# Optimization experiments

Measured on AMD Instinct MI355X. Metric: run time of the kernel, lower is better.

The kernel has to match this reference:

```python
import jax, jax.numpy as jnp
import numpy as np

N_QUBITS = 4
N_LAYERS = 2


def _ry(theta):
    # PennyLane RY(theta) = [[cos(t/2), -sin(t/2)], [sin(t/2), cos(t/2)]]
    c = jnp.cos(theta / 2)
    s = jnp.sin(theta / 2)
    return jnp.stack([jnp.stack([c, -s]), jnp.stack([s, c])]).astype(jnp.complex64)


def _rz(theta):
    # PennyLane RZ(theta) = diag(exp(-i t/2), exp(+i t/2))
    e = jnp.exp(-0.5j * theta.astype(jnp.complex64))
    return jnp.diag(jnp.stack([e, jnp.conj(e)]))


def _apply_1q(state, U, wire):
    # state: (2,)*N_QUBITS complex; contract U into axis `wire`
    state = jnp.tensordot(U, state, axes=((1,), (wire,)))
    return jnp.moveaxis(state, 0, wire)


def _cnot(state, ctrl, tgt):
    s = jnp.moveaxis(state, ctrl, 0)
    t2 = tgt - 1 if tgt > ctrl else tgt
    s1 = jnp.flip(s[1], axis=t2)  # X on target where control == 1
    return jnp.moveaxis(jnp.stack([s[0], s1]), 0, ctrl)


def _circuit(angles, weights):
    # angles: (N_QUBITS,), weights: (N_LAYERS, N_QUBITS, 2)
    state = jnp.zeros((2,) * N_QUBITS, jnp.complex64).at[(0,) * N_QUBITS].set(1.0)
    for i in range(N_QUBITS):
        state = _apply_1q(state, _ry(angles[i]), i)
    for l in range(N_LAYERS):
        for i in range(N_QUBITS):
            state = _apply_1q(state, _ry(weights[l, i, 0]), i)
            state = _apply_1q(state, _rz(weights[l, i, 1]), i)
        for i in range(N_QUBITS - 1):
            state = _cnot(state, i, i + 1)
        state = _cnot(state, N_QUBITS - 1, 0)
    probs = jnp.abs(state) ** 2
    p = probs.reshape(2, -1).sum(axis=1)  # marginal on wire 0
    return p[0] - p[1]  # <Z_0>


def setup_inputs() -> dict:
    key = jax.random.key(0)
    ks = jax.random.split(key, 6)
    B = 65536
    return {
        "x": jax.random.normal(ks[0], (B, 256), jnp.float32),
        "W1": jax.random.normal(ks[1], (64, 256), jnp.float32) * 0.0625,
        "b1": jax.random.normal(ks[2], (64,), jnp.float32) * 0.01,
        "W2": jax.random.normal(ks[3], (4, 64), jnp.float32) * 0.125,
        "b2": jax.random.normal(ks[4], (4,), jnp.float32) * 0.01,
        "q_weights": jax.random.normal(ks[5], (N_LAYERS, N_QUBITS, 2), jnp.float32) * 0.1,
    }


def reference(x, W1, b1, W2, b2, q_weights):
    h = jax.nn.relu(x @ W1.T + b1)          # [B, 64]
    angles = jnp.tanh(h @ W2.T + b2)         # [B, 4]
    z = jax.vmap(lambda a: _circuit(a, q_weights))(angles)  # [B]
    return z[:, None]                        # [B, 1]
```

## Files before the change

kernel.cpp:

```cpp
#include <hip/hip_runtime.h>
#include <math.h>

typedef _Float16 half8  __attribute__((ext_vector_type(8)));
typedef _Float16 half4v __attribute__((ext_vector_type(4)));
typedef float    float4v __attribute__((ext_vector_type(4)));

#define BM   128
#define KDIM 256
#define BKF  128
#define XSTR 136
#define HSW  65

__global__ __launch_bounds__(256, 2)
void qc_fused(const float* __restrict__ x,
              const float* __restrict__ W1,
              const float* __restrict__ b1,
              const float* __restrict__ W2,
              const float* __restrict__ b2,
              const float* __restrict__ qw,
              float* __restrict__ out)
{
    __shared__ _Float16 xh[BM * XSTR];
    __shared__ _Float16 wh[64 * XSTR];
    __shared__ float w2s[256];
    __shared__ float b1s[64];
    __shared__ float b2s[4];
    __shared__ float trig[32];

    const int tid  = threadIdx.x;
    const int lane = tid & 63;
    const int wv   = tid >> 6;
    const int m    = lane & 15;
    const int q    = lane >> 4;
    const int row0 = blockIdx.x * BM;

    w2s[tid] = W2[tid];
    if (tid < 64) b1s[tid] = b1[tid];
    if (tid < 4)  b2s[tid] = b2[tid];
    if (tid < 8) {
        int l = tid >> 2, i = tid & 3;
        float wy = qw[(l * 4 + i) * 2 + 0];
        float wz = qw[(l * 4 + i) * 2 + 1];
        float sy, cy, sz, cz;
        sincosf(0.5f * wy, &sy, &cy);
        sincosf(0.5f * wz, &sz, &cz);
        trig[(l * 4 + i) * 4 + 0] = cy;
        trig[(l * 4 + i) * 4 + 1] = sy;
        trig[(l * 4 + i) * 4 + 2] = cz;
        trig[(l * 4 + i) * 4 + 3] = sz;
    }

    float4v acc[2][4] = {};

    const int sr  = tid >> 3, skq = tid & 7;
    const int wr  = tid >> 2, wkq = tid & 3;

    for (int kc = 0; kc < KDIM; kc += BKF) {
        if (kc) __syncthreads();
        #pragma unroll
        for (int i = 0; i < 4; ++i) {
            #pragma unroll
            for (int j = 0; j < 4; ++j) {
                int row = sr + 32 * i;
                int kf  = 4 * skq + 32 * j;
                const float4v v = *(const float4v*)(x + (size_t)(row0 + row) * KDIM + kc + kf);
                half4v h;
                h[0] = (_Float16)v[0]; h[1] = (_Float16)v[1];
                h[2] = (_Float16)v[2]; h[3] = (_Float16)v[3];
                *(half4v*)&xh[row * XSTR + kf] = h;
            }
        }
        #pragma unroll
        for (int j = 0; j < 8; ++j) {
            int kf = 4 * wkq + 16 * j;
            const float4v v = *(const float4v*)(W1 + (size_t)wr * KDIM + kc + kf);
            half4v h;
            h[0] = (_Float16)v[0]; h[1] = (_Float16)v[1];
            h[2] = (_Float16)v[2]; h[3] = (_Float16)v[3];
            *(half4v*)&wh[wr * XSTR + kf] = h;
        }
        __syncthreads();
        #pragma unroll
        for (int ks = 0; ks < 4; ++ks) {
            const int ko = ks * 32 + q * 8;
            half8 af0 = *(const half8*)&xh[(wv * 32 +      m) * XSTR + ko];
            half8 af1 = *(const half8*)&xh[(wv * 32 + 16 + m) * XSTR + ko];
            #pragma unroll
            for (int b = 0; b < 4; ++b) {
                half8 bf = *(const half8*)&wh[(16 * b + m) * XSTR + ko];
                acc[0][b] = __builtin_amdgcn_mfma_f32_16x16x32_f16(af0, bf, acc[0][b], 0, 0, 0);
                acc[1][b] = __builtin_amdgcn_mfma_f32_16x16x32_f16(af1, bf, acc[1][b], 0, 0, 0);
            }
        }
    }
    __syncthreads();

    float* hs = (float*)xh;
    #pragma unroll
    for (int a = 0; a < 2; ++a) {
        #pragma unroll
        for (int b = 0; b < 4; ++b) {
            #pragma unroll
            for (int i = 0; i < 4; ++i) {
                int row = wv * 32 + 16 * a + 4 * q + i;
                int col = 16 * b + m;
                float v = acc[a][b][i] + b1s[col];
                hs[row * HSW + col] = fmaxf(v, 0.0f);
            }
        }
    }
    __syncthreads();

    if (tid < BM) {
        const int r = tid;
        float s0 = b2s[0], s1 = b2s[1], s2 = b2s[2], s3 = b2s[3];
        #pragma unroll 8
        for (int k = 0; k < 64; ++k) {
            float hv = hs[r * HSW + k];
            s0 = fmaf(hv, w2s[0 * 64 + k], s0);
            s1 = fmaf(hv, w2s[1 * 64 + k], s1);
            s2 = fmaf(hv, w2s[2 * 64 + k], s2);
            s3 = fmaf(hv, w2s[3 * 64 + k], s3);
        }
        float ang[4] = { tanhf(s0), tanhf(s1), tanhf(s2), tanhf(s3) };

        float ca[4], sa[4];
        #pragma unroll
        for (int i = 0; i < 4; ++i)
            __sincosf(0.5f * ang[i], &sa[i], &ca[i]);

        float re[16], im[16];
        #pragma unroll
        for (int idx = 0; idx < 16; ++idx) {
            re[idx] = (idx & 8 ? sa[0] : ca[0]) * (idx & 4 ? sa[1] : ca[1]) *
                      (idx & 2 ? sa[2] : ca[2]) * (idx & 1 ? sa[3] : ca[3]);
            im[idx] = 0.0f;
        }
        #pragma unroll
        for (int l = 0; l < 2; ++l) {
            #pragma unroll
            for (int i = 0; i < 4; ++i) {
                const float cy = trig[(l * 4 + i) * 4 + 0];
                const float sy = trig[(l * 4 + i) * 4 + 1];
                const float cz = trig[(l * 4 + i) * 4 + 2];
                const float sz = trig[(l * 4 + i) * 4 + 3];
                const int mq = 8 >> i;
                #pragma unroll
                for (int idx = 0; idx < 16; ++idx) {
                    if (!(idx & mq)) {
                        int j = idx | mq;
                        float ar = re[idx], ai = im[idx], br = re[j], bi = im[j];
                        re[idx] = fmaf(cy, ar, -sy * br);
                        im[idx] = fmaf(cy, ai, -sy * bi);
                        re[j]   = fmaf(sy, ar,  cy * br);
                        im[j]   = fmaf(sy, ai,  cy * bi);
                    }
                }
                #pragma unroll
                for (int idx = 0; idx < 16; ++idx) {
                    float sgn = (idx & mq) ? sz : -sz;
                    float ar = re[idx], ai = im[idx];
                    re[idx] = fmaf(ar, cz, -ai * sgn);
                    im[idx] = fmaf(ar, sgn, ai * cz);
                }
            }
            #pragma unroll
            for (int c = 0; c < 4; ++c) {
                int t  = (c + 1) & 3;
                int mc = 8 >> c, mt = 8 >> t;
                #pragma unroll
                for (int idx = 0; idx < 16; ++idx) {
                    if ((idx & mc) && !(idx & mt)) {
                        int j = idx | mt;
                        float tr = re[idx]; re[idx] = re[j]; re[j] = tr;
                        float ti = im[idx]; im[idx] = im[j]; im[j] = ti;
                    }
                }
            }
        }
        float z = 0.0f;
        #pragma unroll
        for (int idx = 0; idx < 16; ++idx) {
            float p = re[idx] * re[idx] + im[idx] * im[idx];
            z += (idx & 8) ? -p : p;
        }
        out[row0 + r] = z;
    }
}

extern "C" void kernel_launch(void* const* d_in, const int* in_sizes, int n_in,
                              void* d_out, int out_size, void* d_ws, size_t ws_size,
                              hipStream_t stream) {
    const float* x  = (const float*)d_in[0];
    const float* W1 = (const float*)d_in[1];
    const float* b1 = (const float*)d_in[2];
    const float* W2 = (const float*)d_in[3];
    const float* b2 = (const float*)d_in[4];
    const float* qw = (const float*)d_in[5];
    float* out = (float*)d_out;
    const int B = in_sizes[0] / KDIM;
    qc_fused<<<B / BM, 256, 0, stream>>>(x, W1, b1, W2, b2, qw, out);
}
```

Before: 104.5 us.

## Load x straight into MFMA A-fragments, shrink tile to 64 rows, split second layer across threads

Each wave now reads its 16 rows of x directly from global memory into registers as fp16 A-fragments, so x no longer passes through shared memory. W1 is staged once with the full K, which removes the two-chunk K loop. The block tile shrinks to 64 rows, shared memory is aliased between W1 and the hidden buffer, and occupancy is raised to 4 blocks per SM. The second linear layer is split so all 256 threads each compute one output angle instead of 128 threads computing four. This trades more blocks, and more W1 reloads per row of output, for fewer LDS round trips and fewer idle threads.

Result: slower. 107.6 us (+3.0%).

```diff
diff --git a/kernel.cpp b/kernel.cpp
--- a/kernel.cpp
+++ b/kernel.cpp
@@ -1,17 +1,16 @@
 #include <hip/hip_runtime.h>
 #include <math.h>
 
-typedef _Float16 half8  __attribute__((ext_vector_type(8)));
-typedef _Float16 half4v __attribute__((ext_vector_type(4)));
+typedef _Float16 half8   __attribute__((ext_vector_type(8)));
+typedef _Float16 half4v  __attribute__((ext_vector_type(4)));
 typedef float    float4v __attribute__((ext_vector_type(4)));
 
-#define BM   128
-#define KDIM 256
-#define BKF  128
-#define XSTR 136
-#define HSW  65
-
-__global__ __launch_bounds__(256, 2)
+#define BM    64
+#define KDIM  256
+#define WSTR  264
+#define HSW   65
+
+__global__ __launch_bounds__(256, 4)
 void qc_fused(const float* __restrict__ x,
               const float* __restrict__ W1,
               const float* __restrict__ b1,
@@ -20,12 +19,15 @@
               const float* __restrict__ qw,
               float* __restrict__ out)
 {
-    __shared__ _Float16 xh[BM * XSTR];
-    __shared__ _Float16 wh[64 * XSTR];
+    __shared__ __align__(16) unsigned char smem_raw[BM * WSTR * 2];
     __shared__ float w2s[256];
     __shared__ float b1s[64];
     __shared__ float b2s[4];
     __shared__ float trig[32];
+    __shared__ float angs[BM * 4];
+
+    _Float16* wh = (_Float16*)smem_raw;
+    float*    hs = (float*)smem_raw;
 
     const int tid  = threadIdx.x;
     const int lane = tid & 63;
@@ -33,6 +35,14 @@
     const int m    = lane & 15;
     const int q    = lane >> 4;
     const int row0 = blockIdx.x * BM;
+
+    const float* xrow = x + (size_t)(row0 + wv * 16 + m) * KDIM + q * 8;
+    float4v xv[16];
+    #pragma unroll
+    for (int f = 0; f < 8; ++f) {
+        xv[2 * f]     = *(const float4v*)(xrow + f * 32);
+        xv[2 * f + 1] = *(const float4v*)(xrow + f * 32 + 4);
+    }
 
     w2s[tid] = W2[tid];
     if (tid < 64) b1s[tid] = b1[tid];
@@ -50,84 +60,73 @@
         trig[(l * 4 + i) * 4 + 3] = sz;
     }
 
-    float4v acc[2][4] = {};
-
-    const int sr  = tid >> 3, skq = tid & 7;
-    const int wr  = tid >> 2, wkq = tid & 3;
-
-    for (int kc = 0; kc < KDIM; kc += BKF) {
-        if (kc) __syncthreads();
-        #pragma unroll
-        for (int i = 0; i < 4; ++i) {
-            #pragma unroll
-            for (int j = 0; j < 4; ++j) {
-                int row = sr + 32 * i;
-                int kf  = 4 * skq + 32 * j;
-                const float4v v = *(const float4v*)(x + (size_t)(row0 + row) * KDIM + kc + kf);
-                half4v h;
-                h[0] = (_Float16)v[0]; h[1] = (_Float16)v[1];
-                h[2] = (_Float16)v[2]; h[3] = (_Float16)v[3];
-                *(half4v*)&xh[row * XSTR + kf] = h;
-            }
-        }
-        #pragma unroll
-        for (int j = 0; j < 8; ++j) {
-            int kf = 4 * wkq + 16 * j;
-            const float4v v = *(const float4v*)(W1 + (size_t)wr * KDIM + kc + kf);
+    {
+        const int rw = tid >> 2;
+        const int c0 = (tid & 3) * 4;
+        const float* wrow = W1 + (size_t)rw * KDIM;
+        #pragma unroll
+        for (int j = 0; j < 16; ++j) {
+            float4v v = *(const float4v*)(wrow + c0 + 16 * j);
             half4v h;
             h[0] = (_Float16)v[0]; h[1] = (_Float16)v[1];
             h[2] = (_Float16)v[2]; h[3] = (_Float16)v[3];
-            *(half4v*)&wh[wr * XSTR + kf] = h;
-        }
-        __syncthreads();
-        #pragma unroll
-        for (int ks = 0; ks < 4; ++ks) {
-            const int ko = ks * 32 + q * 8;
-            half8 af0 = *(const half8*)&xh[(wv * 32 +      m) * XSTR + ko];
-            half8 af1 = *(const half8*)&xh[(wv * 32 + 16 + m) * XSTR + ko];
-            #pragma unroll
-            for (int b = 0; b < 4; ++b) {
-                half8 bf = *(const half8*)&wh[(16 * b + m) * XSTR + ko];
-                acc[0][b] = __builtin_amdgcn_mfma_f32_16x16x32_f16(af0, bf, acc[0][b], 0, 0, 0);
-                acc[1][b] = __builtin_amdgcn_mfma_f32_16x16x32_f16(af1, bf, acc[1][b], 0, 0, 0);
-            }
-        }
-    }
-    __syncthreads();
-
-    float* hs = (float*)xh;
-    #pragma unroll
-    for (int a = 0; a < 2; ++a) {
+            *(half4v*)&wh[rw * WSTR + c0 + 16 * j] = h;
+        }
+    }
+
+    half8 afr[8];
+    #pragma unroll
+    for (int f = 0; f < 8; ++f) {
+        afr[f][0] = (_Float16)xv[2 * f][0];
+        afr[f][1] = (_Float16)xv[2 * f][1];
+        afr[f][2] = (_Float16)xv[2 * f][2];
+        afr[f][3] = (_Float16)xv[2 * f][3];
+        afr[f][4] = (_Float16)xv[2 * f + 1][0];
+        afr[f][5] = (_Float16)xv[2 * f + 1][1];
+        afr[f][6] = (_Float16)xv[2 * f + 1][2];
+        afr[f][7] = (_Float16)xv[2 * f + 1][3];
+    }
+
+    __syncthreads();
+
+    float4v acc[4] = {};
+    #pragma unroll
+    for (int f = 0; f < 8; ++f) {
+        const int ko = f * 32 + q * 8;
         #pragma unroll
         for (int b = 0; b < 4; ++b) {
-            #pragma unroll
-            for (int i = 0; i < 4; ++i) {
-                int row = wv * 32 + 16 * a + 4 * q + i;
-                int col = 16 * b + m;
-                float v = acc[a][b][i] + b1s[col];
-                hs[row * HSW + col] = fmaxf(v, 0.0f);
-            }
-        }
-    }
-    __syncthreads();
-
-    if (tid < BM) {
-        const int r = tid;
-        float s0 = b2s[0], s1 = b2s[1], s2 = b2s[2], s3 = b2s[3];
+            half8 bf = *(const half8*)&wh[(16 * b + m) * WSTR + ko];
+            acc[b] = __builtin_amdgcn_mfma_f32_16x16x32_f16(afr[f], bf, acc[b], 0, 0, 0);
+        }
+    }
+    __syncthreads();
+
+    #pragma unroll
+    for (int b = 0; b < 4; ++b) {
+        #pragma unroll
+        for (int i = 0; i < 4; ++i) {
+            int row = wv * 16 + q * 4 + i;
+            int col = 16 * b + m;
+            hs[row * HSW + col] = fmaxf(acc[b][i] + b1s[col], 0.0f);
+        }
+    }
+    __syncthreads();
+
+    {
+        int r = tid & 63, qi = tid >> 6;
+        float s = b2s[qi];
         #pragma unroll 8
-        for (int k = 0; k < 64; ++k) {
-            float hv = hs[r * HSW + k];
-            s0 = fmaf(hv, w2s[0 * 64 + k], s0);
-            s1 = fmaf(hv, w2s[1 * 64 + k], s1);
-            s2 = fmaf(hv, w2s[2 * 64 + k], s2);
-            s3 = fmaf(hv, w2s[3 * 64 + k], s3);
-        }
-        float ang[4] = { tanhf(s0), tanhf(s1), tanhf(s2), tanhf(s3) };
-
+        for (int k = 0; k < 64; ++k)
+            s = fmaf(hs[r * HSW + k], w2s[qi * 64 + k], s);
+        angs[r * 4 + qi] = tanhf(s);
+    }
+    __syncthreads();
+
+    if (tid < 64) {
         float ca[4], sa[4];
         #pragma unroll
         for (int i = 0; i < 4; ++i)
-            __sincosf(0.5f * ang[i], &sa[i], &ca[i]);
+            __sincosf(0.5f * angs[tid * 4 + i], &sa[i], &ca[i]);
 
         float re[16], im[16];
         #pragma unroll
@@ -184,7 +183,7 @@
             float p = re[idx] * re[idx] + im[idx] * im[idx];
             z += (idx & 8) ? -p : p;
         }
-        out[row0 + r] = z;
+        out[row0 + tid] = z;
     }
 }
 
```
